# Optimization experiments

Measured on AMD Instinct MI355X. Metric: run time of the kernel, lower is better.

Reference implementation:

```python
import jax, jax.numpy as jnp
import numpy as np

B, S, H, NH, L = 2, 1024, 512, 8, 4
HD = H // NH
MLP = 4 * H
OUT = 128
SPARSITY = 0.8
EPS = 1e-5


def _pos_encoding(seq_len, d_model):
    pos = jnp.arange(seq_len, dtype=jnp.float32)[:, None]                     # [S,1]
    div = jnp.exp(jnp.arange(0, d_model, 2, dtype=jnp.float32) * (-np.log(10000.0) / d_model))
    ang = pos * div                                                            # [S,D/2]
    pe = jnp.stack([jnp.sin(ang), jnp.cos(ang)], axis=-1).reshape(seq_len, d_model)
    return pe[None]                                                            # [1,S,D]


def _layer_norm(x, g, b):
    m = jnp.mean(x, axis=-1, keepdims=True)
    v = jnp.mean(jnp.square(x - m), axis=-1, keepdims=True)
    return (x - m) * jax.lax.rsqrt(v + EPS) * g + b


def setup_inputs() -> dict:
    key = jax.random.key(0)
    ks = iter(jax.random.split(key, 16))
    w = lambda k, shp: jax.random.normal(k, shp, dtype=jnp.float32) * 0.02
    inp = {
        "x": jax.random.normal(next(ks), (B, S), dtype=jnp.float32),
        "in_w": w(next(ks), (1, H)), "in_b": jnp.zeros((H,), jnp.float32),
        "ln1_g": jnp.ones((L, H), jnp.float32), "ln1_b": jnp.zeros((L, H), jnp.float32),
        "qw": w(next(ks), (L, H, H)), "qb": jnp.zeros((L, H), jnp.float32),
        "kw": w(next(ks), (L, H, H)), "kb": jnp.zeros((L, H), jnp.float32),
        "vw": w(next(ks), (L, H, H)), "vb": jnp.zeros((L, H), jnp.float32),
        "ow": w(next(ks), (L, H, H)), "ob": jnp.zeros((L, H), jnp.float32),
        "ln2_g": jnp.ones((L, H), jnp.float32), "ln2_b": jnp.zeros((L, H), jnp.float32),
        "w1": w(next(ks), (L, H, MLP)), "b1": jnp.zeros((L, MLP), jnp.float32),
        "w2": w(next(ks), (L, MLP, H)), "b2": jnp.zeros((L, H), jnp.float32),
        "fn_g": jnp.ones((H,), jnp.float32), "fn_b": jnp.zeros((H,), jnp.float32),
        "out_w": w(next(ks), (H, OUT)), "out_b": jnp.zeros((OUT,), jnp.float32),
    }
    return inp


def _forward(x, in_w, in_b, ln1_g, ln1_b, qw, qb, kw, kb, vw, vb, ow, ob,
             ln2_g, ln2_b, w1, b1, w2, b2, fn_g, fn_b, out_w, out_b):
    seq_len = x.shape[1]
    k_top = max(1, int(seq_len * (1.0 - SPARSITY)))  # static
    scale = HD ** -0.5

    h = x[..., None] @ in_w + in_b                    # [B,S,H] (input_proj on [B,S,1])
    h = h + _pos_encoding(seq_len, H)

    layer_params = (ln1_g, ln1_b, qw, qb, kw, kb, vw, vb, ow, ob,
                    ln2_g, ln2_b, w1, b1, w2, b2)

    def block(h, p):
        (g1, bb1, Wq, bq, Wk, bk, Wv, bv, Wo, bo, g2, bb2, W1, B1, W2, B2) = p
        n = _layer_norm(h, g1, bb1)
        # project and split heads: [B,S,H] -> [B,NH,S,HD]
        def heads(W, b):
            y = n @ W + b
            return y.reshape(B, seq_len, NH, HD).transpose(0, 2, 1, 3)
        q, k, v = heads(Wq, bq), heads(Wk, bk), heads(Wv, bv)
        scores = jnp.einsum('bhqd,bhkd->bhqk', q, k) * scale
        # top-k sparsification: keep entries >= k-th largest per row (-inf elsewhere)
        kth = jax.lax.top_k(scores, k_top)[0][..., -1:]
        sparse = jnp.where(scores >= kth, scores, -jnp.inf)
        attn = jax.nn.softmax(sparse, axis=-1)
        o = jnp.einsum('bhqk,bhkd->bhqd', attn, v)
        o = o.transpose(0, 2, 1, 3).reshape(B, seq_len, H)
        h = h + (o @ Wo + bo)
        m = _layer_norm(h, g2, bb2)
        m = jax.nn.gelu(m @ W1 + B1, approximate=False) @ W2 + B2
        return h + m, attn

    h, attn_stack = jax.lax.scan(block, h, layer_params)
    out = _layer_norm(h, fn_g, fn_b) @ out_w + out_b  # [B,S,OUT]
    return out, attn_stack                            # attn_stack: [L,B,NH,S,S]


def reference(x, in_w, in_b, ln1_g, ln1_b, qw, qb, kw, kb, vw, vb, ow, ob,
              ln2_g, ln2_b, w1, b1, w2, b2, fn_g, fn_b, out_w, out_b):
    return _forward(x, in_w, in_b, ln1_g, ln1_b, qw, qb, kw, kb, vw, vb, ow, ob,
                    ln2_g, ln2_b, w1, b1, w2, b2, fn_g, fn_b, out_w, out_b)
```

## Files before the change

kernel.cpp:

```cpp
#include <hip/hip_runtime.h>
#include <math.h>

#define DEVINL __device__ __forceinline__

constexpr int S_   = 1024;
constexpr int H_   = 512;
constexpr int NH_  = 8;
constexpr int L_   = 4;
constexpr int HD_  = 64;
constexpr int MLP_ = 2048;
constexpr int OUT_ = 128;
constexpr int B_   = 2;
constexpr int BS_  = 2048;
constexpr int KTOP_ = 204;

typedef __bf16 bf16x8 __attribute__((ext_vector_type(8)));
typedef float f32x4 __attribute__((ext_vector_type(4)));

DEVINL unsigned short f2b(float f) {
  unsigned int u = __float_as_uint(f);
  unsigned int r = (u + 0x7fffu + ((u >> 16) & 1u)) >> 16;
  return (unsigned short)r;
}

DEVINL void gload16(const unsigned short* g, unsigned short* l) {
  __builtin_amdgcn_global_load_lds(
      (const __attribute__((address_space(1))) unsigned int*)g,
      (__attribute__((address_space(3))) unsigned int*)l,
      16, 0, 0);
}

__global__ __launch_bounds__(256) void prep_kernel(
    const float* __restrict__ qw, const float* __restrict__ kw,
    const float* __restrict__ vw, const float* __restrict__ ow,
    const float* __restrict__ w1, const float* __restrict__ w2,
    const float* __restrict__ outw,
    const float* __restrict__ x, const float* __restrict__ in_w,
    const float* __restrict__ in_b,
    unsigned short* __restrict__ Wqkvt, unsigned short* __restrict__ Wot,
    unsigned short* __restrict__ W1t, unsigned short* __restrict__ W2t,
    unsigned short* __restrict__ OWt, float* __restrict__ h)
{
  const int bid = blockIdx.x;
  if (bid >= 12352) {
    const int idx = bid - 12352;
    const int row = idx * 2 + (threadIdx.x >> 7);
    const int s = row & (S_ - 1);
    const int c = (threadIdx.x & 127) * 4;
    const float xv = x[row];
    const float4 wv = *(const float4*)(in_w + c);
    const float4 bv = *(const float4*)(in_b + c);
    const float* wp = (const float*)&wv;
    const float* bp = (const float*)&bv;
    float o[4];
#pragma unroll
    for (int j = 0; j < 4; j++) {
      const int cc = c + j;
      const float di = expf(-(float)(cc & ~1) * (9.210340371976184f / 512.0f));
      const float ang = (float)s * di;
      const float pe = (cc & 1) ? cosf(ang) : sinf(ang);
      o[j] = xv * wp[j] + bp[j] + pe;
    }
    *(float4*)(h + (size_t)row * H_ + c) = make_float4(o[0], o[1], o[2], o[3]);
    return;
  }
  const float* src; unsigned short* dst; int R, C, cx, ry;
  if (bid < 4096) {
    const int z = bid >> 8, rem = bid & 255;
    const int which = z >> 2, l = z & 3;
    src = (which == 0 ? qw : which == 1 ? kw : which == 2 ? vw : ow)
          + (size_t)l * 512 * 512;
    dst = (which < 3)
        ? (Wqkvt + (size_t)l * 1536 * 512 + (size_t)which * 512 * 512)
        : (Wot + (size_t)l * 512 * 512);
    R = 512; C = 512; cx = rem & 15; ry = rem >> 4;
  } else if (bid < 8192) {
    const int idx = bid - 4096, z = idx >> 10, rem = idx & 1023;
    src = w1 + (size_t)z * 512 * 2048;
    dst = W1t + (size_t)z * 2048 * 512;
    R = 512; C = 2048; cx = rem & 63; ry = rem >> 6;
  } else if (bid < 12288) {
    const int idx = bid - 8192, z = idx >> 10, rem = idx & 1023;
    src = w2 + (size_t)z * 2048 * 512;
    dst = W2t + (size_t)z * 512 * 2048;
    R = 2048; C = 512; cx = rem & 15; ry = rem >> 4;
  } else {
    const int idx = bid - 12288;
    src = outw; dst = OWt;
    R = 512; C = 128; cx = idx & 3; ry = idx >> 2;
  }
  __shared__ float tile[32][33];
  const int c0 = cx * 32, r0 = ry * 32;
  const int tx = threadIdx.x & 31, ty = threadIdx.x >> 5;
#pragma unroll
  for (int j = 0; j < 4; j++)
    tile[ty + j * 8][tx] = src[(size_t)(r0 + ty + j * 8) * C + c0 + tx];
  __syncthreads();
#pragma unroll
  for (int j = 0; j < 4; j++)
    dst[(size_t)(c0 + ty + j * 8) * R + r0 + tx] = f2b(tile[tx][ty + j * 8]);
}

__global__ __launch_bounds__(128) void ln_kernel(
    const float* __restrict__ hin, const float* __restrict__ g,
    const float* __restrict__ b, unsigned short* __restrict__ nout)
{
  const int row = blockIdx.x;
  const int t = threadIdx.x;
  const int wid = t >> 6, ln_ = t & 63;
  __shared__ float red[2];
  float4 v = ((const float4*)(hin + (size_t)row * H_))[t];
  float sm = v.x + v.y + v.z + v.w;
#pragma unroll
  for (int m = 1; m < 64; m <<= 1) sm += __shfl_xor(sm, m);
  if (ln_ == 0) red[wid] = sm;
  __syncthreads();
  const float mean = (red[0] + red[1]) * (1.0f / 512.0f);
  __syncthreads();
  const float dx = v.x - mean, dy = v.y - mean, dz = v.z - mean, dw = v.w - mean;
  float ss = dx * dx + dy * dy + dz * dz + dw * dw;
#pragma unroll
  for (int m = 1; m < 64; m <<= 1) ss += __shfl_xor(ss, m);
  if (ln_ == 0) red[wid] = ss;
  __syncthreads();
  const float var = (red[0] + red[1]) * (1.0f / 512.0f);
  const float rs = rsqrtf(var + 1e-5f);
  const float4 gv = ((const float4*)g)[t];
  const float4 bv = ((const float4*)b)[t];
  ushort4 o;
  o.x = f2b(dx * rs * gv.x + bv.x);
  o.y = f2b(dy * rs * gv.y + bv.y);
  o.z = f2b(dz * rs * gv.z + bv.z);
  o.w = f2b(dw * rs * gv.w + bv.w);
  ((ushort4*)(nout + (size_t)row * H_))[t] = o;
}

template <int EPI>
__global__ __launch_bounds__(256, 2) void gemm_kernel(
    const unsigned short* __restrict__ A, const unsigned short* __restrict__ Bt,
    const float* __restrict__ bias, void* __restrict__ Cout,
    int M, int N, int Klen, int Kstride,
    const float* __restrict__ bias2, const float* __restrict__ bias3,
    void* __restrict__ C2, void* __restrict__ C3)
{
  __shared__ unsigned short Alds[2][128 * 32];
  __shared__ unsigned short Blds[2][128 * 32];
  const int tid = threadIdx.x;
  const int w = tid >> 6, lane = tid & 63, lr = lane & 15, lg = lane >> 4;
  const int m0 = blockIdx.x * 128, n0 = blockIdx.y * 128;
  const int wm = (w >> 1) * 64, wn = (w & 1) * 64;

  A  += (size_t)blockIdx.z * Klen;
  Bt += (size_t)blockIdx.z * Klen;

  const int srow = w * 32 + (lane >> 2);
  const int scol = (lane & 3) * 8;
  const unsigned short* Ag0 = A + (size_t)(m0 + srow) * Kstride + scol;
  const unsigned short* Ag1 = A + (size_t)(m0 + srow + 16) * Kstride + scol;
  const unsigned short* Bg0 = Bt + (size_t)(n0 + srow) * Kstride + scol;
  const unsigned short* Bg1 = Bt + (size_t)(n0 + srow + 16) * Kstride + scol;
  const int l0 = (w * 32) * 32;
  const int l1 = (w * 32 + 16) * 32;

  auto STAGE = [&](int buf, int kt) {
    gload16(Ag0 + kt, &Alds[buf][l0]);
    gload16(Ag1 + kt, &Alds[buf][l1]);
    gload16(Bg0 + kt, &Blds[buf][l0]);
    gload16(Bg1 + kt, &Blds[buf][l1]);
  };

  const f32x4 zero4 = {0.f, 0.f, 0.f, 0.f};
  f32x4 acc[4][4];
#pragma unroll
  for (int i = 0; i < 4; i++)
#pragma unroll
    for (int j = 0; j < 4; j++) acc[i][j] = zero4;

  const int nsteps = Klen >> 5;
  STAGE(0, 0);
  __syncthreads();
  int cur = 0;
  for (int t = 0; t < nsteps; t++) {
    if (t + 1 < nsteps) STAGE(cur ^ 1, (t + 1) * 32);
    bf16x8 af[4], bfr[4];
#pragma unroll
    for (int mi = 0; mi < 4; mi++)
      af[mi] = *(const bf16x8*)(&Alds[cur][(wm + mi * 16 + lr) * 32 + lg * 8]);
#pragma unroll
    for (int ni = 0; ni < 4; ni++)
      bfr[ni] = *(const bf16x8*)(&Blds[cur][(wn + ni * 16 + lr) * 32 + lg * 8]);
#pragma unroll
    for (int mi = 0; mi < 4; mi++)
#pragma unroll
      for (int ni = 0; ni < 4; ni++)
        acc[mi][ni] = __builtin_amdgcn_mfma_f32_16x16x32_bf16(af[mi], bfr[ni], acc[mi][ni], 0, 0, 0);
    __syncthreads();
    cur ^= 1;
  }

#pragma unroll
  for (int mi = 0; mi < 4; mi++) {
#pragma unroll
    for (int ni = 0; ni < 4; ni++) {
      const int col = n0 + wn + ni * 16 + lr;
      if constexpr (EPI == 5) {
        if (col < 512) {
          const float bs = bias[col];
#pragma unroll
          for (int r = 0; r < 4; r++) {
            const int row = m0 + wm + mi * 16 + lg * 4 + r;
            ((unsigned short*)Cout)[(size_t)row * 512 + col] =
                f2b((acc[mi][ni][r] + bs) * 0.125f);
          }
        } else if (col < 1024) {
          const float bs = bias2[col - 512];
#pragma unroll
          for (int r = 0; r < 4; r++) {
            const int row = m0 + wm + mi * 16 + lg * 4 + r;
            ((unsigned short*)C2)[(size_t)row * 512 + (col - 512)] =
                f2b(acc[mi][ni][r] + bs);
          }
        } else {
          const float bs = bias3[col - 1024];
          const int row0_ = m0 + wm + mi * 16 + lg * 4;
          const int bb = row0_ >> 10, ssi = row0_ & 1023;
          ushort4 pk;
          pk.x = f2b(acc[mi][ni][0] + bs);
          pk.y = f2b(acc[mi][ni][1] + bs);
          pk.z = f2b(acc[mi][ni][2] + bs);
          pk.w = f2b(acc[mi][ni][3] + bs);
          *(ushort4*)((unsigned short*)C3 + ((size_t)(bb * 512 + (col - 1024))) * 1024 + ssi) = pk;
        }
      } else if constexpr (EPI == 6) {
        const float bs = (blockIdx.z == 0) ? bias[col] : 0.f;
#pragma unroll
        for (int r = 0; r < 4; r++) {
          const int row = m0 + wm + mi * 16 + lg * 4 + r;
          atomicAdd(&((float*)Cout)[(size_t)row * N + col], acc[mi][ni][r] + bs);
        }
      } else {
        const float bs = bias[col];
#pragma unroll
        for (int r = 0; r < 4; r++) {
          const int row = m0 + wm + mi * 16 + lg * 4 + r;
          float val = acc[mi][ni][r] + bs;
          const size_t idx = (size_t)row * N + col;
          if constexpr (EPI == 2) {
            val = 0.5f * val * (1.0f + erff(val * 0.7071067811865475f));
            ((unsigned short*)Cout)[idx] = f2b(val);
          } else {
            ((float*)Cout)[idx] = val;
          }
        }
      }
    }
  }
}

__global__ __launch_bounds__(256, 2) void attn_fused_kernel(
    const unsigned short* __restrict__ qbf, const unsigned short* __restrict__ kbf,
    const unsigned short* __restrict__ vt, float* __restrict__ attnL,
    unsigned short* __restrict__ obf)
{
  constexpr int LDF = 1032;
  __shared__ float sc[16 * LDF];
  const int mblk = blockIdx.x, bnh = blockIdx.y;
  const int b = bnh >> 3, nh = bnh & 7;
  const int tid = threadIdx.x, w = tid >> 6, lane = tid & 63;
  const int lr = lane & 15, lg = lane >> 4;
  const int row0 = mblk * 16;

  const unsigned short* qbase = qbf + ((size_t)(b * S_ + row0)) * H_ + nh * HD_;
  const unsigned short* kbase = kbf + (size_t)(b * S_) * H_ + nh * HD_;

  const f32x4 zero4 = {0.f, 0.f, 0.f, 0.f};

  {
    f32x4 acc[16];
#pragma unroll
    for (int kt = 0; kt < 16; kt++) acc[kt] = zero4;
    bf16x8 qf[2];
    qf[0] = *(const bf16x8*)(qbase + (size_t)lr * H_ + lg * 8);
    qf[1] = *(const bf16x8*)(qbase + (size_t)lr * H_ + 32 + lg * 8);
    const int kw0 = w * 256;
#pragma unroll
    for (int kt = 0; kt < 16; kt++) {
      const unsigned short* kp = kbase + (size_t)(kw0 + kt * 16 + lr) * H_ + lg * 8;
      const bf16x8 kf0 = *(const bf16x8*)(kp);
      const bf16x8 kf1 = *(const bf16x8*)(kp + 32);
      acc[kt] = __builtin_amdgcn_mfma_f32_16x16x32_bf16(kf0, qf[0], acc[kt], 0, 0, 0);
      acc[kt] = __builtin_amdgcn_mfma_f32_16x16x32_bf16(kf1, qf[1], acc[kt], 0, 0, 0);
    }
#pragma unroll
    for (int kt = 0; kt < 16; kt++)
      *(f32x4*)(sc + (size_t)lr * LDF + kw0 + kt * 16 + lg * 4) = acc[kt];
  }
  __syncthreads();

#pragma unroll 1
  for (int rr = 0; rr < 4; rr++) {
    const int row = w * 4 + rr;
    float* rowp = sc + (size_t)row * LDF;
    float v[16];
#pragma unroll
    for (int j = 0; j < 8; j++) {
      const float2 t2 = *(const float2*)(rowp + 2 * lane + j * 128);
      v[2 * j] = t2.x; v[2 * j + 1] = t2.y;
    }
    unsigned int keys[16];
#pragma unroll
    for (int j = 0; j < 16; j++) {
      const unsigned int u = __float_as_uint(v[j]);
      keys[j] = (u & 0x80000000u) ? ~u : (u | 0x80000000u);
    }
    unsigned int prefix = 0u;
#pragma unroll 1
    for (int bit = 31; bit >= 0; bit--) {
      const unsigned int cand = prefix | (1u << bit);
      int cnt = 0;
#pragma unroll
      for (int j = 0; j < 16; j++)
        cnt += (int)__popcll(__ballot(keys[j] >= cand));
      if (cnt >= KTOP_) prefix = cand;
    }
    const unsigned int fb = (prefix & 0x80000000u) ? (prefix & 0x7fffffffu) : ~prefix;
    const float thresh = __uint_as_float(fb);

    float mx = v[0];
#pragma unroll
    for (int j = 1; j < 16; j++) mx = fmaxf(mx, v[j]);
#pragma unroll
    for (int m = 1; m < 64; m <<= 1) mx = fmaxf(mx, __shfl_xor(mx, m));
    float p[16];
    float ssum = 0.f;
#pragma unroll
    for (int j = 0; j < 16; j++) {
      const float e = expf(v[j] - mx);
      p[j] = (v[j] >= thresh) ? e : 0.f;
      ssum += p[j];
    }
#pragma unroll
    for (int m = 1; m < 64; m <<= 1) ssum += __shfl_xor(ssum, m);
    const float inv = 1.0f / ssum;
    float* outrow = attnL + (size_t)bnh * S_ * S_ + (size_t)(row0 + row) * S_;
    unsigned short* prow = (unsigned short*)rowp;
#pragma unroll
    for (int j = 0; j < 8; j++) {
      const float p0 = p[2 * j] * inv, p1 = p[2 * j + 1] * inv;
      *(float2*)(outrow + 2 * lane + j * 128) = make_float2(p0, p1);
      const unsigned int pk = ((unsigned int)f2b(p1) << 16) | (unsigned int)f2b(p0);
      *(unsigned int*)(prow + 2 * lane + j * 128) = pk;
    }
  }
  __syncthreads();

  const unsigned short* vb = vt + (size_t)(b * 512 + nh * HD_) * S_;
  f32x4 oacc[4];
#pragma unroll
  for (int ni = 0; ni < 4; ni++) oacc[ni] = zero4;
  const unsigned short* scu = (const unsigned short*)sc;
#pragma unroll
  for (int ks = 0; ks < 8; ks++) {
    const int k0 = w * 256 + ks * 32;
    const bf16x8 pf = *(const bf16x8*)(scu + (size_t)lr * (2 * LDF) + k0 + lg * 8);
    bf16x8 vfr[4];
#pragma unroll
    for (int ni = 0; ni < 4; ni++)
      vfr[ni] = *(const bf16x8*)(vb + (size_t)(ni * 16 + lr) * S_ + k0 + lg * 8);
#pragma unroll
    for (int ni = 0; ni < 4; ni++)
      oacc[ni] = __builtin_amdgcn_mfma_f32_16x16x32_bf16(pf, vfr[ni], oacc[ni], 0, 0, 0);
  }
  __syncthreads();
  float* red = sc + w * 1024;
#pragma unroll
  for (int ni = 0; ni < 4; ni++)
#pragma unroll
    for (int r = 0; r < 4; r++)
      red[(lg * 4 + r) * 64 + ni * 16 + lr] = oacc[ni][r];
  __syncthreads();
  {
    const int orow = tid >> 4, oc0 = (tid & 15) * 4;
    const float* rp = sc + orow * 64 + oc0;
    float4 s0 = *(const float4*)rp;
#pragma unroll
    for (int ww = 1; ww < 4; ww++) {
      const float4 a = *(const float4*)(rp + ww * 1024);
      s0.x += a.x; s0.y += a.y; s0.z += a.z; s0.w += a.w;
    }
    ushort4 o1;
    o1.x = f2b(s0.x); o1.y = f2b(s0.y); o1.z = f2b(s0.z); o1.w = f2b(s0.w);
    unsigned short* dst = obf + (size_t)(b * S_ + row0 + orow) * H_ + nh * HD_ + oc0;
    *(ushort4*)dst = o1;
  }
}

extern "C" void kernel_launch(void* const* d_in, const int* in_sizes, int n_in,
                              void* d_out, int out_size, void* d_ws, size_t ws_size,
                              hipStream_t stream)
{
  (void)in_sizes; (void)n_in; (void)out_size; (void)ws_size;
  const float* x     = (const float*)d_in[0];
  const float* in_w  = (const float*)d_in[1];
  const float* in_b  = (const float*)d_in[2];
  const float* ln1_g = (const float*)d_in[3];
  const float* ln1_b = (const float*)d_in[4];
  const float* qw    = (const float*)d_in[5];
  const float* qbias = (const float*)d_in[6];
  const float* kw    = (const float*)d_in[7];
  const float* kbias = (const float*)d_in[8];
  const float* vw    = (const float*)d_in[9];
  const float* vbias = (const float*)d_in[10];
  const float* ow    = (const float*)d_in[11];
  const float* obias = (const float*)d_in[12];
  const float* ln2_g = (const float*)d_in[13];
  const float* ln2_b = (const float*)d_in[14];
  const float* w1    = (const float*)d_in[15];
  const float* b1    = (const float*)d_in[16];
  const float* w2    = (const float*)d_in[17];
  const float* b2    = (const float*)d_in[18];
  const float* fn_g  = (const float*)d_in[19];
  const float* fn_b  = (const float*)d_in[20];
  const float* out_w = (const float*)d_in[21];
  const float* out_b = (const float*)d_in[22];

  char* ws = (char*)d_ws;
  size_t off = 0;
  auto alloc = [&](size_t bytes) -> void* {
    void* p = ws + off;
    off += (bytes + 255) & ~(size_t)255;
    return p;
  };
  float* h             = (float*)alloc((size_t)BS_ * H_ * 4);
  unsigned short* Wqkvt = (unsigned short*)alloc((size_t)L_ * 1536 * H_ * 2);
  unsigned short* Wot  = (unsigned short*)alloc((size_t)L_ * H_ * H_ * 2);
  unsigned short* W1t  = (unsigned short*)alloc((size_t)L_ * MLP_ * H_ * 2);
  unsigned short* W2t  = (unsigned short*)alloc((size_t)L_ * H_ * MLP_ * 2);
  unsigned short* OWt  = (unsigned short*)alloc((size_t)OUT_ * H_ * 2);
  unsigned short* nbf  = (unsigned short*)alloc((size_t)BS_ * H_ * 2);
  unsigned short* qbf  = (unsigned short*)alloc((size_t)BS_ * H_ * 2);
  unsigned short* kbf  = (unsigned short*)alloc((size_t)BS_ * H_ * 2);
  unsigned short* vtb  = (unsigned short*)alloc((size_t)B_ * 512 * S_ * 2);
  unsigned short* obf  = (unsigned short*)alloc((size_t)BS_ * H_ * 2);
  unsigned short* tbf  = (unsigned short*)alloc((size_t)BS_ * MLP_ * 2);

  float* attn_base = (float*)d_out + (size_t)BS_ * OUT_;

  const dim3 tb(256);
  prep_kernel<<<dim3(13376), tb, 0, stream>>>(
      qw, kw, vw, ow, w1, w2, out_w, x, in_w, in_b,
      Wqkvt, Wot, W1t, W2t, OWt, h);

  for (int l = 0; l < L_; l++) {
    float* attnL = attn_base + (size_t)l * 16 * S_ * S_;
    ln_kernel<<<dim3(BS_), dim3(128), 0, stream>>>(h, ln1_g + l * H_, ln1_b + l * H_, nbf);
    gemm_kernel<5><<<dim3(16, 12), tb, 0, stream>>>(
        nbf, Wqkvt + (size_t)l * 1536 * H_, qbias + l * H_, qbf, BS_, 1536, H_, H_,
        kbias + l * H_, vbias + l * H_, kbf, vtb);
    attn_fused_kernel<<<dim3(64, 16), tb, 0, stream>>>(qbf, kbf, vtb, attnL, obf);
    gemm_kernel<6><<<dim3(16, 4, 2), tb, 0, stream>>>(
        obf, Wot + (size_t)l * H_ * H_, obias + l * H_, h, BS_, H_, 256, H_,
        nullptr, nullptr, nullptr, nullptr);
    ln_kernel<<<dim3(BS_), dim3(128), 0, stream>>>(h, ln2_g + l * H_, ln2_b + l * H_, nbf);
    gemm_kernel<2><<<dim3(16, 16), tb, 0, stream>>>(
        nbf, W1t + (size_t)l * MLP_ * H_, b1 + l * MLP_, tbf, BS_, MLP_, H_, H_,
        nullptr, nullptr, nullptr, nullptr);
    gemm_kernel<6><<<dim3(16, 4, 4), tb, 0, stream>>>(
        tbf, W2t + (size_t)l * H_ * MLP_, b2 + l * H_, h, BS_, H_, 512, MLP_,
        nullptr, nullptr, nullptr, nullptr);
  }

  ln_kernel<<<dim3(BS_), dim3(128), 0, stream>>>(h, fn_g, fn_b, nbf);
  gemm_kernel<3><<<dim3(16, 1), tb, 0, stream>>>(
      nbf, OWt, out_b, d_out, BS_, OUT_, H_, H_,
      nullptr, nullptr, nullptr, nullptr);
}
```

Measured before the change: 1.035 ms.

## Fuse LayerNorm into GEMM A-loading and replace split-K atomics with residual add

```diff
diff --git a/kernel.cpp b/kernel.cpp
--- a/kernel.cpp
+++ b/kernel.cpp
@@ -101,72 +101,77 @@
     dst[(size_t)(c0 + ty + j * 8) * R + r0 + tx] = f2b(tile[tx][ty + j * 8]);
 }
 
-__global__ __launch_bounds__(128) void ln_kernel(
-    const float* __restrict__ hin, const float* __restrict__ g,
-    const float* __restrict__ b, unsigned short* __restrict__ nout)
-{
-  const int row = blockIdx.x;
-  const int t = threadIdx.x;
-  const int wid = t >> 6, ln_ = t & 63;
-  __shared__ float red[2];
-  float4 v = ((const float4*)(hin + (size_t)row * H_))[t];
-  float sm = v.x + v.y + v.z + v.w;
-#pragma unroll
-  for (int m = 1; m < 64; m <<= 1) sm += __shfl_xor(sm, m);
-  if (ln_ == 0) red[wid] = sm;
-  __syncthreads();
-  const float mean = (red[0] + red[1]) * (1.0f / 512.0f);
-  __syncthreads();
-  const float dx = v.x - mean, dy = v.y - mean, dz = v.z - mean, dw = v.w - mean;
-  float ss = dx * dx + dy * dy + dz * dz + dw * dw;
-#pragma unroll
-  for (int m = 1; m < 64; m <<= 1) ss += __shfl_xor(ss, m);
-  if (ln_ == 0) red[wid] = ss;
-  __syncthreads();
-  const float var = (red[0] + red[1]) * (1.0f / 512.0f);
-  const float rs = rsqrtf(var + 1e-5f);
-  const float4 gv = ((const float4*)g)[t];
-  const float4 bv = ((const float4*)b)[t];
-  ushort4 o;
-  o.x = f2b(dx * rs * gv.x + bv.x);
-  o.y = f2b(dy * rs * gv.y + bv.y);
-  o.z = f2b(dz * rs * gv.z + bv.z);
-  o.w = f2b(dw * rs * gv.w + bv.w);
-  ((ushort4*)(nout + (size_t)row * H_))[t] = o;
-}
-
 template <int EPI>
-__global__ __launch_bounds__(256, 2) void gemm_kernel(
-    const unsigned short* __restrict__ A, const unsigned short* __restrict__ Bt,
-    const float* __restrict__ bias, void* __restrict__ Cout,
-    int M, int N, int Klen, int Kstride,
+__global__ __launch_bounds__(256, 2) void gemm_ln_kernel(
+    const float* __restrict__ hsrc, const unsigned short* __restrict__ Bt,
+    const float* __restrict__ g, const float* __restrict__ b,
+    const float* __restrict__ bias, void* __restrict__ Cout, int N,
     const float* __restrict__ bias2, const float* __restrict__ bias3,
     void* __restrict__ C2, void* __restrict__ C3)
 {
-  __shared__ unsigned short Alds[2][128 * 32];
+  constexpr int LDA = 40;
+  __shared__ unsigned short Albuf[2][128 * LDA];
   __shared__ unsigned short Blds[2][128 * 32];
+  __shared__ float gbl[1024];
   const int tid = threadIdx.x;
   const int w = tid >> 6, lane = tid & 63, lr = lane & 15, lg = lane >> 4;
   const int m0 = blockIdx.x * 128, n0 = blockIdx.y * 128;
   const int wm = (w >> 1) * 64, wn = (w & 1) * 64;
 
-  A  += (size_t)blockIdx.z * Klen;
-  Bt += (size_t)blockIdx.z * Klen;
+  const int rt = tid >> 1, hf = tid & 1;
+  const float* hrow = hsrc + (size_t)(m0 + rt) * 512 + hf * 256;
+  float s1 = 0.f, s2 = 0.f;
+#pragma unroll 8
+  for (int j = 0; j < 64; j++) {
+    const float4 v = ((const float4*)hrow)[j];
+    s1 += v.x + v.y + v.z + v.w;
+    s2 += v.x * v.x + v.y * v.y + v.z * v.z + v.w * v.w;
+  }
+  s1 += __shfl_xor(s1, 1);
+  s2 += __shfl_xor(s2, 1);
+  const float mean = s1 * (1.0f / 512.0f);
+  const float var = s2 * (1.0f / 512.0f) - mean * mean;
+  const float rs = rsqrtf(var + 1e-5f);
+
+  *(float2*)&gbl[tid * 2] = *(const float2*)&g[tid * 2];
+  *(float2*)&gbl[512 + tid * 2] = *(const float2*)&b[tid * 2];
 
   const int srow = w * 32 + (lane >> 2);
   const int scol = (lane & 3) * 8;
-  const unsigned short* Ag0 = A + (size_t)(m0 + srow) * Kstride + scol;
-  const unsigned short* Ag1 = A + (size_t)(m0 + srow + 16) * Kstride + scol;
-  const unsigned short* Bg0 = Bt + (size_t)(n0 + srow) * Kstride + scol;
-  const unsigned short* Bg1 = Bt + (size_t)(n0 + srow + 16) * Kstride + scol;
-  const int l0 = (w * 32) * 32;
-  const int l1 = (w * 32 + 16) * 32;
-
-  auto STAGE = [&](int buf, int kt) {
-    gload16(Ag0 + kt, &Alds[buf][l0]);
-    gload16(Ag1 + kt, &Alds[buf][l1]);
-    gload16(Bg0 + kt, &Blds[buf][l0]);
-    gload16(Bg1 + kt, &Blds[buf][l1]);
+  const unsigned short* Bg0 = Bt + (size_t)(n0 + srow) * 512 + scol;
+  const unsigned short* Bg1 = Bt + (size_t)(n0 + srow + 16) * 512 + scol;
+  const int bl0 = (w * 32) * 32;
+  const int bl1 = (w * 32 + 16) * 32;
+
+  float ar[16];
+  auto ALOAD = [&](int t) {
+    const float* p = hsrc + (size_t)(m0 + rt) * 512 + t * 32 + hf * 16;
+#pragma unroll
+    for (int i = 0; i < 4; i++) {
+      const float4 v = ((const float4*)p)[i];
+      ar[i * 4 + 0] = v.x; ar[i * 4 + 1] = v.y;
+      ar[i * 4 + 2] = v.z; ar[i * 4 + 3] = v.w;
+    }
+  };
+  auto AWRITE = [&](int buf, int t) {
+    const int c0 = t * 32 + hf * 16;
+    unsigned short tmp[16];
+#pragma unroll
+    for (int i = 0; i < 4; i++) {
+      const f32x4 gv = *(const f32x4*)&gbl[c0 + i * 4];
+      const f32x4 bv = *(const f32x4*)&gbl[512 + c0 + i * 4];
+#pragma unroll
+      for (int j = 0; j < 4; j++)
+        tmp[i * 4 + j] = f2b((ar[i * 4 + j] - mean) * rs * gv[j] + bv[j]);
+    }
+    unsigned short* d = &Albuf[buf][rt * LDA + hf * 16];
+    *(int4*)d = *(const int4*)tmp;
+    *(int4*)(d + 8) = *(const int4*)(tmp + 8);
+  };
+  auto STAGE_B = [&](int buf, int t) {
+    const int kt = t * 32;
+    gload16(Bg0 + kt, &Blds[buf][bl0]);
+    gload16(Bg1 + kt, &Blds[buf][bl1]);
   };
 
   const f32x4 zero4 = {0.f, 0.f, 0.f, 0.f};
@@ -176,16 +181,21 @@
 #pragma unroll
     for (int j = 0; j < 4; j++) acc[i][j] = zero4;
 
-  const int nsteps = Klen >> 5;
-  STAGE(0, 0);
+  __syncthreads();
+  ALOAD(0);
+  AWRITE(0, 0);
+  STAGE_B(0, 0);
   __syncthreads();
   int cur = 0;
-  for (int t = 0; t < nsteps; t++) {
-    if (t + 1 < nsteps) STAGE(cur ^ 1, (t + 1) * 32);
+  for (int t = 0; t < 16; t++) {
+    if (t + 1 < 16) {
+      ALOAD(t + 1);
+      STAGE_B(cur ^ 1, t + 1);
+    }
     bf16x8 af[4], bfr[4];
 #pragma unroll
     for (int mi = 0; mi < 4; mi++)
-      af[mi] = *(const bf16x8*)(&Alds[cur][(wm + mi * 16 + lr) * 32 + lg * 8]);
+      af[mi] = *(const bf16x8*)(&Albuf[cur][(wm + mi * 16 + lr) * LDA + lg * 8]);
 #pragma unroll
     for (int ni = 0; ni < 4; ni++)
       bfr[ni] = *(const bf16x8*)(&Blds[cur][(wn + ni * 16 + lr) * 32 + lg * 8]);
@@ -194,6 +204,7 @@
 #pragma unroll
       for (int ni = 0; ni < 4; ni++)
         acc[mi][ni] = __builtin_amdgcn_mfma_f32_16x16x32_bf16(af[mi], bfr[ni], acc[mi][ni], 0, 0, 0);
+    if (t + 1 < 16) AWRITE(cur ^ 1, t + 1);
     __syncthreads();
     cur ^= 1;
   }
@@ -231,13 +242,6 @@
           pk.w = f2b(acc[mi][ni][3] + bs);
           *(ushort4*)((unsigned short*)C3 + ((size_t)(bb * 512 + (col - 1024))) * 1024 + ssi) = pk;
         }
-      } else if constexpr (EPI == 6) {
-        const float bs = (blockIdx.z == 0) ? bias[col] : 0.f;
-#pragma unroll
-        for (int r = 0; r < 4; r++) {
-          const int row = m0 + wm + mi * 16 + lg * 4 + r;
-          atomicAdd(&((float*)Cout)[(size_t)row * N + col], acc[mi][ni][r] + bs);
-        }
       } else {
         const float bs = bias[col];
 #pragma unroll
@@ -252,6 +256,78 @@
             ((float*)Cout)[idx] = val;
           }
         }
+      }
+    }
+  }
+}
+
+__global__ __launch_bounds__(256, 2) void gemm_res_kernel(
+    const unsigned short* __restrict__ A, const unsigned short* __restrict__ Bt,
+    const float* __restrict__ bias, float* __restrict__ Cout,
+    int N, int K)
+{
+  __shared__ unsigned short Alds[2][128 * 32];
+  __shared__ unsigned short Blds[2][128 * 32];
+  const int tid = threadIdx.x;
+  const int w = tid >> 6, lane = tid & 63, lr = lane & 15, lg = lane >> 4;
+  const int m0 = blockIdx.x * 128, n0 = blockIdx.y * 128;
+  const int wm = (w >> 1) * 64, wn = (w & 1) * 64;
+
+  const int srow = w * 32 + (lane >> 2);
+  const int scol = (lane & 3) * 8;
+  const unsigned short* Ag0 = A + (size_t)(m0 + srow) * K + scol;
+  const unsigned short* Ag1 = A + (size_t)(m0 + srow + 16) * K + scol;
+  const unsigned short* Bg0 = Bt + (size_t)(n0 + srow) * K + scol;
+  const unsigned short* Bg1 = Bt + (size_t)(n0 + srow + 16) * K + scol;
+  const int l0 = (w * 32) * 32;
+  const int l1 = (w * 32 + 16) * 32;
+
+  auto STAGE = [&](int buf, int kt) {
+    gload16(Ag0 + kt, &Alds[buf][l0]);
+    gload16(Ag1 + kt, &Alds[buf][l1]);
+    gload16(Bg0 + kt, &Blds[buf][l0]);
+    gload16(Bg1 + kt, &Blds[buf][l1]);
+  };
+
+  const f32x4 zero4 = {0.f, 0.f, 0.f, 0.f};
+  f32x4 acc[4][4];
+#pragma unroll
+  for (int i = 0; i < 4; i++)
+#pragma unroll
+    for (int j = 0; j < 4; j++) acc[i][j] = zero4;
+
+  const int nsteps = K >> 5;
+  STAGE(0, 0);
+  __syncthreads();
+  int cur = 0;
+  for (int t = 0; t < nsteps; t++) {
+    if (t + 1 < nsteps) STAGE(cur ^ 1, (t + 1) * 32);
+    bf16x8 af[4], bfr[4];
+#pragma unroll
+    for (int mi = 0; mi < 4; mi++)
+      af[mi] = *(const bf16x8*)(&Alds[cur][(wm + mi * 16 + lr) * 32 + lg * 8]);
+#pragma unroll
+    for (int ni = 0; ni < 4; ni++)
+      bfr[ni] = *(const bf16x8*)(&Blds[cur][(wn + ni * 16 + lr) * 32 + lg * 8]);
+#pragma unroll
+    for (int mi = 0; mi < 4; mi++)
+#pragma unroll
+      for (int ni = 0; ni < 4; ni++)
+        acc[mi][ni] = __builtin_amdgcn_mfma_f32_16x16x32_bf16(af[mi], bfr[ni], acc[mi][ni], 0, 0, 0);
+    __syncthreads();
+    cur ^= 1;
+  }
+
+#pragma unroll
+  for (int mi = 0; mi < 4; mi++) {
+#pragma unroll
+    for (int ni = 0; ni < 4; ni++) {
+      const int col = n0 + wn + ni * 16 + lr;
+      const float bs = bias[col];
+#pragma unroll
+      for (int r = 0; r < 4; r++) {
+        const int row = m0 + wm + mi * 16 + lg * 4 + r;
+        Cout[(size_t)row * N + col] += acc[mi][ni][r] + bs;
       }
     }
   }
@@ -437,7 +513,6 @@
   unsigned short* W1t  = (unsigned short*)alloc((size_t)L_ * MLP_ * H_ * 2);
   unsigned short* W2t  = (unsigned short*)alloc((size_t)L_ * H_ * MLP_ * 2);
   unsigned short* OWt  = (unsigned short*)alloc((size_t)OUT_ * H_ * 2);
-  unsigned short* nbf  = (unsigned short*)alloc((size_t)BS_ * H_ * 2);
   unsigned short* qbf  = (unsigned short*)alloc((size_t)BS_ * H_ * 2);
   unsigned short* kbf  = (unsigned short*)alloc((size_t)BS_ * H_ * 2);
   unsigned short* vtb  = (unsigned short*)alloc((size_t)B_ * 512 * S_ * 2);
@@ -453,25 +528,22 @@
 
   for (int l = 0; l < L_; l++) {
     float* attnL = attn_base + (size_t)l * 16 * S_ * S_;
-    ln_kernel<<<dim3(BS_), dim3(128), 0, stream>>>(h, ln1_g + l * H_, ln1_b + l * H_, nbf);
-    gemm_kernel<5><<<dim3(16, 12), tb, 0, stream>>>(
-        nbf, Wqkvt + (size_t)l * 1536 * H_, qbias + l * H_, qbf, BS_, 1536, H_, H_,
+    gemm_ln_kernel<5><<<dim3(16, 12), tb, 0, stream>>>(
+        h, Wqkvt + (size_t)l * 1536 * H_, ln1_g + l * H_, ln1_b + l * H_,
+        qbias + l * H_, qbf, 1536,
         kbias + l * H_, vbias + l * H_, kbf, vtb);
     attn_fused_kernel<<<dim3(64, 16), tb, 0, stream>>>(qbf, kbf, vtb, attnL, obf);
-    gemm_kernel<6><<<dim3(16, 4, 2), tb, 0, stream>>>(
-        obf, Wot + (size_t)l * H_ * H_, obias + l * H_, h, BS_, H_, 256, H_,
+    gemm_res_kernel<<<dim3(16, 4), tb, 0, stream>>>(
+        obf, Wot + (size_t)l * H_ * H_, obias + l * H_, h, H_, H_);
+    gemm_ln_kernel<2><<<dim3(16, 16), tb, 0, stream>>>(
+        h, W1t + (size_t)l * MLP_ * H_, ln2_g + l * H_, ln2_b + l * H_,
+        b1 + l * MLP_, tbf, MLP_,
         nullptr, nullptr, nullptr, nullptr);
-    ln_kernel<<<dim3(BS_), dim3(128), 0, stream>>>(h, ln2_g + l * H_, ln2_b + l * H_, nbf);
-    gemm_kernel<2><<<dim3(16, 16), tb, 0, stream>>>(
-        nbf, W1t + (size_t)l * MLP_ * H_, b1 + l * MLP_, tbf, BS_, MLP_, H_, H_,
-        nullptr, nullptr, nullptr, nullptr);
-    gemm_kernel<6><<<dim3(16, 4, 4), tb, 0, stream>>>(
-        tbf, W2t + (size_t)l * H_ * MLP_, b2 + l * H_, h, BS_, H_, 512, MLP_,
-        nullptr, nullptr, nullptr, nullptr);
-  }
-
-  ln_kernel<<<dim3(BS_), dim3(128), 0, stream>>>(h, fn_g, fn_b, nbf);
-  gemm_kernel<3><<<dim3(16, 1), tb, 0, stream>>>(
-      nbf, OWt, out_b, d_out, BS_, OUT_, H_, H_,
+    gemm_res_kernel<<<dim3(16, 4), tb, 0, stream>>>(
+        tbf, W2t + (size_t)l * H_ * MLP_, b2 + l * H_, h, H_, MLP_);
+  }
+
+  gemm_ln_kernel<3><<<dim3(16, 1), tb, 0, stream>>>(
+      h, OWt, fn_g, fn_b, out_b, d_out, OUT_,
       nullptr, nullptr, nullptr, nullptr);
 }
```

After: 1.269 ms. 1.23x slower.
